# Optimization experiments

Measured on AMD Instinct MI355X. Metric: run time of the kernel, lower is better.

## Reference

```python
import jax, jax.numpy as jnp
import numpy as np

N_TOKENS = 16384
DIM = 4096
NUM_EXPERTS = 128
TOP_K = 8


def setup_inputs() -> dict:
    key = jax.random.key(0)
    k1, k2 = jax.random.split(key)
    x = jax.random.normal(k1, (N_TOKENS, DIM), dtype=jnp.float32)
    gate_w = jax.random.normal(k2, (NUM_EXPERTS, DIM), dtype=jnp.float32) * (DIM ** -0.5)
    return {"x": x, "gate_w": gate_w, "experts_per_token": TOP_K, "num_experts": NUM_EXPERTS}


def reference(x, gate_w, experts_per_token, num_experts):
    # gate: x @ W^T -> (N, E) logits
    scores = jnp.einsum('nd,ed->ne', x, gate_w)
    # softmax in fp32, cast back to input dtype
    probs = jax.nn.softmax(scores.astype(jnp.float32), axis=-1).astype(x.dtype)
    # stable descending argsort (argsort of negated probs, stable)
    sorted_indices = jnp.argsort(-probs, axis=1, stable=True)
    selected_experts = sorted_indices[:, :experts_per_token]            # (N, k)
    top_scores = jnp.take_along_axis(probs, selected_experts, axis=1)   # (N, k)
    # norm_topk_prob=True: renormalize selected weights to sum to 1
    denom = jnp.clip(top_scores.sum(axis=-1, keepdims=True), 1e-8, None)
    top_scores = top_scores / denom
    flat_experts = selected_experts.reshape(-1)                         # (N*k,)
    num_tokens_per_expert = jnp.bincount(flat_experts, length=num_experts)
    # stable sort token-slots by expert id for expert grouping
    perm = jnp.argsort(flat_experts, stable=True)                       # (N*k,)
    top_scores_sorted = top_scores.reshape(-1)[perm]
    token_indices = perm // experts_per_token
    return top_scores_sorted, token_indices, num_tokens_per_expert
```

## Files before the change

### kernel.cpp

```cpp
#include <hip/hip_runtime.h>
#include <math.h>

typedef _Float16 f16;
typedef f16 f16x8 __attribute__((ext_vector_type(8)));
typedef float f32x4 __attribute__((ext_vector_type(4)));

#define NT    16384
#define DIM   4096
#define NEXP  128
#define TOPK  8
#define NFLAT (NT * TOPK)
#define BT    64
#define NFB   (NT / BT)
#define SBLK  512
#define BK    64
#define NSTEP (DIM / BK)

#define COUNTS_OFF 0
#define SEL_OFF    1024
#define WGT_OFF    (SEL_OFF + NFLAT * 4)
#define BH_OFF     (WGT_OFF + NFLAT * 4)
#define BO_OFF     (BH_OFF + NEXP * SBLK * 4)
#define WPK_OFF    (BO_OFF + NEXP * SBLK * 4)

#define G1P __attribute__((address_space(1)))
#define L3P __attribute__((address_space(3)))

__device__ __forceinline__ void gload_lds16(const void* g, void* l) {
    __builtin_amdgcn_global_load_lds((const G1P unsigned int*)g,
                                     (L3P unsigned int*)l, 16, 0, 0);
}

__device__ __forceinline__ void split2(float v, f16& h, f16& m) {
    h = (f16)v;
    m = (f16)((v - (float)h) * 2048.0f);
}

__global__ __launch_bounds__(256)
void wsplit_kernel(const float* __restrict__ gw, char* __restrict__ wpk) {
    const int t = blockIdx.x * 256 + threadIdx.x;
    const int l = t & 63, kkc = (t >> 6) & 1, g = (t >> 7) & 7, st = t >> 10;
    const int e = g * 16 + (l & 15);
    const int k0 = st * 64 + kkc * 32 + (l >> 4) * 8;
    float4 a = *(const float4*)&gw[e * 4096 + k0];
    float4 b = *(const float4*)&gw[e * 4096 + k0 + 4];
    union { f16 f[8]; uint4 u; } ph, pm;
    split2(a.x * 64.f, ph.f[0], pm.f[0]); split2(a.y * 64.f, ph.f[1], pm.f[1]);
    split2(a.z * 64.f, ph.f[2], pm.f[2]); split2(a.w * 64.f, ph.f[3], pm.f[3]);
    split2(b.x * 64.f, ph.f[4], pm.f[4]); split2(b.y * 64.f, ph.f[5], pm.f[5]);
    split2(b.z * 64.f, ph.f[6], pm.f[6]); split2(b.w * 64.f, ph.f[7], pm.f[7]);
    const size_t base = ((size_t)(st * 8 + g) * 4 + kkc) * 1024 + l * 16;
    *(uint4*)(wpk + base)        = ph.u;
    *(uint4*)(wpk + base + 2048) = pm.u;
}

__global__ __launch_bounds__(512, 2)
void fused_kernel(const float* __restrict__ x, const char* __restrict__ wpk,
                  float* __restrict__ wgt, int* __restrict__ sel,
                  int* __restrict__ counts, int* __restrict__ bh) {
    __shared__ __align__(16) char smem[98304];
    char* WB = smem + 32768;

    const int tid  = threadIdx.x;
    const int tok0 = blockIdx.x * BT;
    const int lane = tid & 63, wid = tid >> 6;
    const int r = wid >> 2, eg = wid & 3;
    const int fr = lane & 15, hi = lane >> 4;
    const int srow = tid >> 3;
    const int skq  = (tid & 7) * 8;
    const int xi = srow >> 4, xfr = srow & 15;
    const int xkk = skq >> 5, xhi = (skq >> 3) & 3;
    const int xslot = xhi * 16 + xfr;
    const int xwb = ((xi * 2 + xkk) * 64 + (xslot ^ ((xslot >> 4) << 1))) * 16;
    const int lxs = (lane ^ ((lane >> 4) << 1)) * 16;
    const int myg = 2 * eg + r;

    f32x4 acc0[2][2], acc1[2][2];
#pragma unroll
    for (int i = 0; i < 2; ++i)
#pragma unroll
        for (int j = 0; j < 2; ++j) {
            acc0[i][j] = (f32x4){0.f, 0.f, 0.f, 0.f};
            acc1[i][j] = (f32x4){0.f, 0.f, 0.f, 0.f};
        }

    const size_t xrow = (size_t)(tok0 + srow) * DIM;

#define X_PREF(RA, RB, SI) { \
    RA = *(const float4*)&x[xrow + (size_t)(SI) * BK + skq]; \
    RB = *(const float4*)&x[xrow + (size_t)(SI) * BK + skq + 4]; }
#define W_PREF(SI, B) { \
    const char* wsrc = wpk + ((size_t)(SI) * 8 + myg) * 4096 + lane * 16; \
    char* wdst = WB + (B) * 32768 + myg * 4096; \
    gload_lds16(wsrc,        wdst); \
    gload_lds16(wsrc + 1024, wdst + 1024); \
    gload_lds16(wsrc + 2048, wdst + 2048); \
    gload_lds16(wsrc + 3072, wdst + 3072); }
#define STAGE(CUR, RA, RB) { \
    union { f16 f[8]; f16x8 v; } ph, pm; \
    split2(RA.x, ph.f[0], pm.f[0]); split2(RA.y, ph.f[1], pm.f[1]); \
    split2(RA.z, ph.f[2], pm.f[2]); split2(RA.w, ph.f[3], pm.f[3]); \
    split2(RB.x, ph.f[4], pm.f[4]); split2(RB.y, ph.f[5], pm.f[5]); \
    split2(RB.z, ph.f[6], pm.f[6]); split2(RB.w, ph.f[7], pm.f[7]); \
    *(f16x8*)(smem + (CUR) * 8192 + xwb) = ph.v; \
    *(f16x8*)(smem + 16384 + (CUR) * 8192 + xwb) = pm.v; }
#define COMPUTE(CUR) { \
    _Pragma("unroll") \
    for (int kk = 0; kk < 2; ++kk) { \
        f16x8 ah[2], am[2], bhf[2], bmf[2]; \
        _Pragma("unroll") \
        for (int i = 0; i < 2; ++i) { \
            const int xb = (CUR) * 8192 + ((2 * r + i) * 2 + kk) * 1024 + lxs; \
            ah[i] = *(const f16x8*)(smem + xb); \
            am[i] = *(const f16x8*)(smem + 16384 + xb); \
        } \
        _Pragma("unroll") \
        for (int j = 0; j < 2; ++j) { \
            const int wb = (CUR) * 32768 + (2 * eg + j) * 4096 + kk * 1024 + lane * 16; \
            bhf[j] = *(const f16x8*)(WB + wb); \
            bmf[j] = *(const f16x8*)(WB + wb + 2048); \
        } \
        _Pragma("unroll") \
        for (int i = 0; i < 2; ++i) \
        _Pragma("unroll") \
        for (int j = 0; j < 2; ++j) { \
            acc0[i][j] = __builtin_amdgcn_mfma_f32_16x16x32_f16(ah[i], bhf[j], acc0[i][j], 0, 0, 0); \
            acc1[i][j] = __builtin_amdgcn_mfma_f32_16x16x32_f16(ah[i], bmf[j], acc1[i][j], 0, 0, 0); \
            acc1[i][j] = __builtin_amdgcn_mfma_f32_16x16x32_f16(am[i], bhf[j], acc1[i][j], 0, 0, 0); \
        } \
    } }
#define STEP(CUR, RA, RB, PX, PW, SI, VMSTR) { \
    STAGE(CUR, RA, RB); \
    asm volatile("s_waitcnt lgkmcnt(0) vmcnt(" VMSTR ")" ::: "memory"); \
    __builtin_amdgcn_s_barrier(); \
    if (PW) { W_PREF((SI) + 1, (CUR) ^ 1); } \
    __builtin_amdgcn_sched_barrier(0); \
    if (PX) { X_PREF(RA, RB, (SI) + 2); } \
    __builtin_amdgcn_s_setprio(1); \
    COMPUTE(CUR); \
    __builtin_amdgcn_s_setprio(0); }

    float4 a0, b0, a1, b1;
    W_PREF(0, 0);
    X_PREF(a0, b0, 0);
    X_PREF(a1, b1, 1);

    for (int st = 0; st < 62; st += 2) {
        STEP(0, a0, b0, 1, 1, st, "2");
        STEP(1, a1, b1, 1, 1, st + 1, "2");
    }
    STEP(0, a0, b0, 0, 1, 62, "2");
    STEP(1, a1, b1, 0, 0, 63, "0");

    __syncthreads();

    float* S  = (float*)smem;
    int*   h2 = (int*)(smem + 34816);
#pragma unroll
    for (int i = 0; i < 2; ++i)
#pragma unroll
        for (int j = 0; j < 2; ++j)
#pragma unroll
            for (int q = 0; q < 4; ++q) {
                int t = r * 32 + i * 16 + hi * 4 + q;
                int e = eg * 32 + j * 16 + fr;
                S[t * 129 + e] =
                    (acc0[i][j][q] + acc1[i][j][q] * (1.0f / 2048.0f)) * (1.0f / 64.0f);
            }
    if (tid < 256) h2[tid] = 0;
    __syncthreads();

    if (tid < BT) {
        float bs[8]; int bi[8];
#pragma unroll
        for (int q = 0; q < 8; ++q) { bs[q] = -3.0e38f; bi[q] = 0; }
        for (int e = 0; e < NEXP; ++e) {
            float s = S[tid * 129 + e];
            if (s > bs[7]) {
                int pos = 7;
#pragma unroll
                for (int q = 6; q >= 0; q--) pos = (s > bs[q]) ? q : pos;
#pragma unroll
                for (int q = 7; q >= 1; q--) {
                    bool sh = (q > pos);
                    bs[q] = sh ? bs[q - 1] : bs[q];
                    bi[q] = sh ? bi[q - 1] : bi[q];
                }
#pragma unroll
                for (int q = 0; q < 8; q++)
                    if (q == pos) { bs[q] = s; bi[q] = e; }
            }
        }
        float m = bs[0], sum = 0.f, ex[8];
#pragma unroll
        for (int q = 0; q < 8; ++q) { ex[q] = expf(bs[q] - m); sum += ex[q]; }
        float inv = 1.f / fmaxf(sum, 1e-8f);
        const int tok = tok0 + tid;
#pragma unroll
        for (int q = 0; q < 8; ++q) {
            wgt[tok * TOPK + q] = ex[q] * inv;
            sel[tok * TOPK + q] = bi[q];
            atomicAdd(&h2[(tid >> 5) * NEXP + bi[q]], 1);
        }
    }
    __syncthreads();
    if (tid < NEXP) {
        int c0 = h2[tid], c1 = h2[NEXP + tid];
        bh[tid * SBLK + 2 * blockIdx.x]     = c0;
        bh[tid * SBLK + 2 * blockIdx.x + 1] = c1;
        if (c0 + c1) atomicAdd(&counts[tid], c0 + c1);
    }
}

__global__ void scan_kernel(const int* __restrict__ bh, const int* __restrict__ counts,
                            int* __restrict__ bo, float* __restrict__ out) {
    const int e = blockIdx.x, tid = threadIdx.x;
    __shared__ int pre[NEXP];
    __shared__ int wsum[8];
    if (tid < NEXP) pre[tid] = counts[tid];
    __syncthreads();
#pragma unroll
    for (int d = 1; d < NEXP; d <<= 1) {
        int o = (tid < NEXP && tid >= d) ? pre[tid - d] : 0;
        __syncthreads();
        if (tid < NEXP) pre[tid] += o;
        __syncthreads();
    }
    const int gb = (e == 0) ? 0 : pre[e - 1];
    if (tid == 0) out[2 * NFLAT + e] = (float)counts[e];

    const int lane = tid & 63, wid = tid >> 6;
    int v = bh[e * SBLK + tid];
    int sc = v;
#pragma unroll
    for (int d = 1; d < 64; d <<= 1) {
        int o = __shfl_up(sc, d);
        sc += (lane >= d) ? o : 0;
    }
    if (lane == 63) wsum[wid] = sc;
    __syncthreads();
    int add = 0;
#pragma unroll
    for (int ww = 0; ww < 8; ww++) add += (ww < wid) ? wsum[ww] : 0;
    bo[e * SBLK + tid] = gb + sc - v + add;
}

__global__ void scatter_kernel(const int* __restrict__ sel, const float* __restrict__ wgt,
                               const int* __restrict__ bo, float* __restrict__ out) {
    const int tid = threadIdx.x, b = blockIdx.x;
    const int i = b * 256 + tid;
    const int e = sel[i];
    const int lane = tid & 63, wid = tid >> 6;
    unsigned long long m = ~0ull;
#pragma unroll
    for (int bit = 0; bit < 7; bit++) {
        unsigned long long bal = __ballot((e >> bit) & 1);
        m &= ((e >> bit) & 1) ? bal : ~bal;
    }
    unsigned long long lower = (lane == 0) ? 0ull : (~0ull >> (64 - lane));
    int wrank = __popcll(m & lower);

    __shared__ int wh_[4][NEXP];
    ((int*)wh_)[tid] = 0; ((int*)wh_)[tid + 256] = 0;
    __syncthreads();
    if (wrank == 0) wh_[wid][e] = __popcll(m);
    __syncthreads();
    int off = 0;
#pragma unroll
    for (int ww = 0; ww < 4; ww++) off += (ww < wid) ? wh_[ww][e] : 0;

    int pos = bo[e * SBLK + b] + off + wrank;
    out[pos] = wgt[i];
    out[NFLAT + pos] = (float)(i >> 3);
}

extern "C" void kernel_launch(void* const* d_in, const int* in_sizes, int n_in,
                              void* d_out, int out_size, void* d_ws, size_t ws_size,
                              hipStream_t stream) {
    const float* x  = (const float*)d_in[0];
    const float* gw = (const float*)d_in[1];
    float* out = (float*)d_out;
    char*  ws  = (char*)d_ws;

    int*   counts = (int*)(ws + COUNTS_OFF);
    int*   sel    = (int*)(ws + SEL_OFF);
    float* wgt    = (float*)(ws + WGT_OFF);
    int*   bh     = (int*)(ws + BH_OFF);
    int*   bo     = (int*)(ws + BO_OFF);
    char*  wpk    = ws + WPK_OFF;

    hipMemsetAsync(counts, 0, NEXP * sizeof(int), stream);

    wsplit_kernel<<<256, 256, 0, stream>>>(gw, wpk);
    fused_kernel<<<NFB, 512, 0, stream>>>(x, wpk, wgt, sel, counts, bh);
    scan_kernel<<<NEXP, 512, 0, stream>>>(bh, counts, bo, out);
    scatter_kernel<<<SBLK, 256, 0, stream>>>(sel, wgt, bo, out);
}
```

Baseline: 118.0 us.

## Shrink token tile to 32 and load gate weights directly into registers

The token tile per block is halved to 32 rows, with 256 threads and about 17 KB of LDS, so more blocks fit per CU and the grid doubles to 512 blocks. Each wave now keeps its split fp16 weight fragments in double-buffered registers loaded straight from global memory, replacing the async global-to-LDS weight staging. This cuts LDS use and barrier-coupled weight traffic. In exchange, each block rereads the full weight matrix, doubling total weight reads from L2, and register pressure rises.

```diff
diff --git a/kernel.cpp b/kernel.cpp
--- a/kernel.cpp
+++ b/kernel.cpp
@@ -10,7 +10,7 @@
 #define NEXP  128
 #define TOPK  8
 #define NFLAT (NT * TOPK)
-#define BT    64
+#define BT    32
 #define NFB   (NT / BT)
 #define SBLK  512
 #define BK    64
@@ -22,14 +22,6 @@
 #define BH_OFF     (WGT_OFF + NFLAT * 4)
 #define BO_OFF     (BH_OFF + NEXP * SBLK * 4)
 #define WPK_OFF    (BO_OFF + NEXP * SBLK * 4)
-
-#define G1P __attribute__((address_space(1)))
-#define L3P __attribute__((address_space(3)))
-
-__device__ __forceinline__ void gload_lds16(const void* g, void* l) {
-    __builtin_amdgcn_global_load_lds((const G1P unsigned int*)g,
-                                     (L3P unsigned int*)l, 16, 0, 0);
-}
 
 __device__ __forceinline__ void split2(float v, f16& h, f16& m) {
     h = (f16)v;
@@ -54,17 +46,15 @@
     *(uint4*)(wpk + base + 2048) = pm.u;
 }
 
-__global__ __launch_bounds__(512, 2)
+__global__ __launch_bounds__(256, 3)
 void fused_kernel(const float* __restrict__ x, const char* __restrict__ wpk,
                   float* __restrict__ wgt, int* __restrict__ sel,
                   int* __restrict__ counts, int* __restrict__ bh) {
-    __shared__ __align__(16) char smem[98304];
-    char* WB = smem + 32768;
+    __shared__ __align__(16) char smem[17408];
 
     const int tid  = threadIdx.x;
     const int tok0 = blockIdx.x * BT;
-    const int lane = tid & 63, wid = tid >> 6;
-    const int r = wid >> 2, eg = wid & 3;
+    const int lane = tid & 63, eg = tid >> 6;
     const int fr = lane & 15, hi = lane >> 4;
     const int srow = tid >> 3;
     const int skq  = (tid & 7) * 8;
@@ -73,7 +63,6 @@
     const int xslot = xhi * 16 + xfr;
     const int xwb = ((xi * 2 + xkk) * 64 + (xslot ^ ((xslot >> 4) << 1))) * 16;
     const int lxs = (lane ^ ((lane >> 4) << 1)) * 16;
-    const int myg = 2 * eg + r;
 
     f32x4 acc0[2][2], acc1[2][2];
 #pragma unroll
@@ -89,85 +78,82 @@
 #define X_PREF(RA, RB, SI) { \
     RA = *(const float4*)&x[xrow + (size_t)(SI) * BK + skq]; \
     RB = *(const float4*)&x[xrow + (size_t)(SI) * BK + skq + 4]; }
-#define W_PREF(SI, B) { \
-    const char* wsrc = wpk + ((size_t)(SI) * 8 + myg) * 4096 + lane * 16; \
-    char* wdst = WB + (B) * 32768 + myg * 4096; \
-    gload_lds16(wsrc,        wdst); \
-    gload_lds16(wsrc + 1024, wdst + 1024); \
-    gload_lds16(wsrc + 2048, wdst + 2048); \
-    gload_lds16(wsrc + 3072, wdst + 3072); }
+#define B_PREF(SI, BH_, BM_) { \
+    const char* wsrc = wpk + ((size_t)(SI) * 8 + 2 * eg) * 4096 + lane * 16; \
+    BH_[0][0] = *(const f16x8*)(wsrc); \
+    BH_[0][1] = *(const f16x8*)(wsrc + 1024); \
+    BM_[0][0] = *(const f16x8*)(wsrc + 2048); \
+    BM_[0][1] = *(const f16x8*)(wsrc + 3072); \
+    BH_[1][0] = *(const f16x8*)(wsrc + 4096); \
+    BH_[1][1] = *(const f16x8*)(wsrc + 5120); \
+    BM_[1][0] = *(const f16x8*)(wsrc + 6144); \
+    BM_[1][1] = *(const f16x8*)(wsrc + 7168); }
 #define STAGE(CUR, RA, RB) { \
     union { f16 f[8]; f16x8 v; } ph, pm; \
     split2(RA.x, ph.f[0], pm.f[0]); split2(RA.y, ph.f[1], pm.f[1]); \
     split2(RA.z, ph.f[2], pm.f[2]); split2(RA.w, ph.f[3], pm.f[3]); \
     split2(RB.x, ph.f[4], pm.f[4]); split2(RB.y, ph.f[5], pm.f[5]); \
     split2(RB.z, ph.f[6], pm.f[6]); split2(RB.w, ph.f[7], pm.f[7]); \
-    *(f16x8*)(smem + (CUR) * 8192 + xwb) = ph.v; \
-    *(f16x8*)(smem + 16384 + (CUR) * 8192 + xwb) = pm.v; }
-#define COMPUTE(CUR) { \
+    *(f16x8*)(smem + (CUR) * 4096 + xwb) = ph.v; \
+    *(f16x8*)(smem + 8192 + (CUR) * 4096 + xwb) = pm.v; }
+#define COMPUTE(CUR, BH_, BM_) { \
     _Pragma("unroll") \
     for (int kk = 0; kk < 2; ++kk) { \
-        f16x8 ah[2], am[2], bhf[2], bmf[2]; \
+        f16x8 ah[2], am[2]; \
         _Pragma("unroll") \
         for (int i = 0; i < 2; ++i) { \
-            const int xb = (CUR) * 8192 + ((2 * r + i) * 2 + kk) * 1024 + lxs; \
+            const int xb = (CUR) * 4096 + (i * 2 + kk) * 1024 + lxs; \
             ah[i] = *(const f16x8*)(smem + xb); \
-            am[i] = *(const f16x8*)(smem + 16384 + xb); \
-        } \
-        _Pragma("unroll") \
-        for (int j = 0; j < 2; ++j) { \
-            const int wb = (CUR) * 32768 + (2 * eg + j) * 4096 + kk * 1024 + lane * 16; \
-            bhf[j] = *(const f16x8*)(WB + wb); \
-            bmf[j] = *(const f16x8*)(WB + wb + 2048); \
+            am[i] = *(const f16x8*)(smem + 8192 + xb); \
         } \
         _Pragma("unroll") \
         for (int i = 0; i < 2; ++i) \
         _Pragma("unroll") \
         for (int j = 0; j < 2; ++j) { \
-            acc0[i][j] = __builtin_amdgcn_mfma_f32_16x16x32_f16(ah[i], bhf[j], acc0[i][j], 0, 0, 0); \
-            acc1[i][j] = __builtin_amdgcn_mfma_f32_16x16x32_f16(ah[i], bmf[j], acc1[i][j], 0, 0, 0); \
-            acc1[i][j] = __builtin_amdgcn_mfma_f32_16x16x32_f16(am[i], bhf[j], acc1[i][j], 0, 0, 0); \
+            acc0[i][j] = __builtin_amdgcn_mfma_f32_16x16x32_f16(ah[i], BH_[j][kk], acc0[i][j], 0, 0, 0); \
+            acc1[i][j] = __builtin_amdgcn_mfma_f32_16x16x32_f16(ah[i], BM_[j][kk], acc1[i][j], 0, 0, 0); \
+            acc1[i][j] = __builtin_amdgcn_mfma_f32_16x16x32_f16(am[i], BH_[j][kk], acc1[i][j], 0, 0, 0); \
         } \
     } }
-#define STEP(CUR, RA, RB, PX, PW, SI, VMSTR) { \
+#define STEP(CUR, RA, RB, BHU, BMU, BHP, BMP, PX, PB, SI) { \
     STAGE(CUR, RA, RB); \
-    asm volatile("s_waitcnt lgkmcnt(0) vmcnt(" VMSTR ")" ::: "memory"); \
+    asm volatile("s_waitcnt lgkmcnt(0)" ::: "memory"); \
     __builtin_amdgcn_s_barrier(); \
-    if (PW) { W_PREF((SI) + 1, (CUR) ^ 1); } \
-    __builtin_amdgcn_sched_barrier(0); \
     if (PX) { X_PREF(RA, RB, (SI) + 2); } \
+    if (PB) { B_PREF((SI) + 1, BHP, BMP); } \
     __builtin_amdgcn_s_setprio(1); \
-    COMPUTE(CUR); \
+    COMPUTE(CUR, BHU, BMU); \
     __builtin_amdgcn_s_setprio(0); }
 
+    f16x8 bhA[2][2], bmA[2][2], bhB[2][2], bmB[2][2];
     float4 a0, b0, a1, b1;
-    W_PREF(0, 0);
+    B_PREF(0, bhA, bmA);
     X_PREF(a0, b0, 0);
     X_PREF(a1, b1, 1);
 
     for (int st = 0; st < 62; st += 2) {
-        STEP(0, a0, b0, 1, 1, st, "2");
-        STEP(1, a1, b1, 1, 1, st + 1, "2");
-    }
-    STEP(0, a0, b0, 0, 1, 62, "2");
-    STEP(1, a1, b1, 0, 0, 63, "0");
-
-    __syncthreads();
-
-    float* S  = (float*)smem;
-    int*   h2 = (int*)(smem + 34816);
+        STEP(0, a0, b0, bhA, bmA, bhB, bmB, 1, 1, st);
+        STEP(1, a1, b1, bhB, bmB, bhA, bmA, 1, 1, st + 1);
+    }
+    STEP(0, a0, b0, bhA, bmA, bhB, bmB, 0, 1, 62);
+    STEP(1, a1, b1, bhB, bmB, bhA, bmA, 0, 0, 63);
+
+    __syncthreads();
+
+    float* S = (float*)smem;
+    int*   h = (int*)(smem + 16512);
 #pragma unroll
     for (int i = 0; i < 2; ++i)
 #pragma unroll
         for (int j = 0; j < 2; ++j)
 #pragma unroll
             for (int q = 0; q < 4; ++q) {
-                int t = r * 32 + i * 16 + hi * 4 + q;
+                int t = i * 16 + hi * 4 + q;
                 int e = eg * 32 + j * 16 + fr;
                 S[t * 129 + e] =
                     (acc0[i][j][q] + acc1[i][j][q] * (1.0f / 2048.0f)) * (1.0f / 64.0f);
             }
-    if (tid < 256) h2[tid] = 0;
+    if (tid < NEXP) h[tid] = 0;
     __syncthreads();
 
     if (tid < BT) {
@@ -200,15 +186,14 @@
         for (int q = 0; q < 8; ++q) {
             wgt[tok * TOPK + q] = ex[q] * inv;
             sel[tok * TOPK + q] = bi[q];
-            atomicAdd(&h2[(tid >> 5) * NEXP + bi[q]], 1);
+            atomicAdd(&h[bi[q]], 1);
         }
     }
     __syncthreads();
     if (tid < NEXP) {
-        int c0 = h2[tid], c1 = h2[NEXP + tid];
-        bh[tid * SBLK + 2 * blockIdx.x]     = c0;
-        bh[tid * SBLK + 2 * blockIdx.x + 1] = c1;
-        if (c0 + c1) atomicAdd(&counts[tid], c0 + c1);
+        int c = h[tid];
+        bh[tid * SBLK + blockIdx.x] = c;
+        if (c) atomicAdd(&counts[tid], c);
     }
 }
 
@@ -292,7 +277,7 @@
     hipMemsetAsync(counts, 0, NEXP * sizeof(int), stream);
 
     wsplit_kernel<<<256, 256, 0, stream>>>(gw, wpk);
-    fused_kernel<<<NFB, 512, 0, stream>>>(x, wpk, wgt, sel, counts, bh);
+    fused_kernel<<<NFB, 256, 0, stream>>>(x, wpk, wgt, sel, counts, bh);
     scan_kernel<<<NEXP, 512, 0, stream>>>(bh, counts, bo, out);
     scatter_kernel<<<SBLK, 256, 0, stream>>>(sel, wgt, bo, out);
 }
```

New measurement: 138.1 us. 1.17x slower.
